# Kernel optimization log

Measured on AMD Instinct MI355X. Metric: run time of the kernel, lower is better.

Reference implementation:

```python
import jax, jax.numpy as jnp
from jax import lax
import numpy as np


def _embed_renorm(table, idx):
    # torch nn.Embedding(max_norm=1): rows with L2 norm > 1 are rescaled to norm 1
    e = table[idx]
    n = jnp.linalg.norm(e, axis=-1, keepdims=True)
    return jnp.where(n > 1.0, e / jnp.maximum(n, 1e-12), e)


def _lstm(x, wih, whh, b, reverse=False):
    # x: [N, T, D]; torch gate order i, f, g, o; zero initial (h, c)
    N, T, _ = x.shape
    H = whh.shape[1]
    xT = jnp.swapaxes(x, 0, 1)  # [T, N, D]
    if reverse:
        xT = xT[::-1]
    pre = jnp.einsum('tnd,gd->tng', xT, wih) + b  # input contribution, [T, N, 4H]

    def step(carry, p):
        h, c = carry
        g = p + h @ whh.T
        i, f, gg, o = jnp.split(g, 4, axis=-1)
        c = jax.nn.sigmoid(f) * c + jax.nn.sigmoid(i) * jnp.tanh(gg)
        h = jax.nn.sigmoid(o) * jnp.tanh(c)
        return (h, c), h

    init = (jnp.zeros((N, H), x.dtype), jnp.zeros((N, H), x.dtype))
    _, hs = lax.scan(step, init, pre)  # [T, N, H]
    if reverse:
        hs = hs[::-1]
    return jnp.swapaxes(hs, 0, 1)  # [N, T, H]


def setup_inputs() -> dict:
    key = jax.random.key(0)
    ks = iter(jax.random.split(key, 32))
    B, W, C = 64, 256, 16
    Vw, Vc, Dw, Dc, H, O = 50000, 100, 256, 64, 512, 3
    s = 0.05  # weight scale to keep LSTM gates in a sane range
    inp = {}
    inp['words'] = jax.random.randint(next(ks), (B, W), 0, Vw)
    inp['chars'] = jax.random.randint(next(ks), (B, W, C), 0, Vc)
    inp['wl_emb'] = jax.random.normal(next(ks), (Vw, Dw), jnp.float32)
    cl_emb = jax.random.normal(next(ks), (Vc, Dc), jnp.float32)
    inp['cl_emb'] = cl_emb.at[0].set(0.0)  # padding_idx=0
    inp['char_wih'] = jax.random.normal(next(ks), (4 * Dc, Dc), jnp.float32) * s
    inp['char_whh'] = jax.random.normal(next(ks), (4 * Dc, Dc), jnp.float32) * s
    inp['char_b'] = jax.random.normal(next(ks), (4 * Dc,), jnp.float32) * s
    for nm in ['l0f', 'l0b']:
        inp[nm + '_wih'] = jax.random.normal(next(ks), (4 * H, Dw + Dc), jnp.float32) * s
        inp[nm + '_whh'] = jax.random.normal(next(ks), (4 * H, H), jnp.float32) * s
        inp[nm + '_b'] = jax.random.normal(next(ks), (4 * H,), jnp.float32) * s
    for nm in ['lf', 'lb']:
        inp[nm + '_wih'] = jax.random.normal(next(ks), (2, 4 * H, 2 * H), jnp.float32) * s
        inp[nm + '_whh'] = jax.random.normal(next(ks), (2, 4 * H, H), jnp.float32) * s
        inp[nm + '_b'] = jax.random.normal(next(ks), (2, 4 * H), jnp.float32) * s
    inp['Wc'] = jax.random.normal(next(ks), (O, 2 * H), jnp.float32) * s
    inp['bc'] = jax.random.normal(next(ks), (O,), jnp.float32) * s
    return inp


def reference(words, chars, wl_emb, cl_emb, char_wih, char_whh, char_b,
              l0f_wih, l0f_whh, l0f_b, l0b_wih, l0b_whh, l0b_b,
              lf_wih, lf_whh, lf_b, lb_wih, lb_whh, lb_b, Wc, bc):
    B, W = words.shape
    C = chars.shape[-1]
    # word-level embeddings
    wl = _embed_renorm(wl_emb, words)  # [B, W, Dw]
    # char-level: batch all B*W ragged words through one LSTM (same math as the
    # per-word python loop: zero-init LSTM per word, take last timestep output)
    ce = _embed_renorm(cl_emb, chars.reshape(B * W, C))  # [B*W, C, Dc]
    ch = _lstm(ce, char_wih, char_whh, char_b)[:, -1, :]  # [B*W, Dc]
    cl = ch.reshape(B, W, -1)
    x = jnp.concatenate([wl, cl], axis=-1)  # [B, W, Dw+Dc]
    # 3-layer bidirectional word LSTM
    h = jnp.concatenate([
        _lstm(x, l0f_wih, l0f_whh, l0f_b),
        _lstm(x, l0b_wih, l0b_whh, l0b_b, reverse=True)], axis=-1)
    for k in range(2):
        h = jnp.concatenate([
            _lstm(h, lf_wih[k], lf_whh[k], lf_b[k]),
            _lstm(h, lb_wih[k], lb_whh[k], lb_b[k], reverse=True)], axis=-1)
    H = h.shape[-1] // 2
    # last_state=True, bi=True: last fwd output + first bwd output
    feat = jnp.concatenate([h[:, -1, :H], h[:, 0, H:]], axis=-1)  # [B, 2H]
    return feat @ Wc.T + bc  # [B, output_size]
```

## Files before the change

### kernel.cpp

```cpp
#include <hip/hip_runtime.h>
#include <math.h>

#define T_   256
#define C_   16

typedef float    f32x4  __attribute__((ext_vector_type(4)));
typedef float    f32x16 __attribute__((ext_vector_type(16)));
typedef _Float16 f16x8  __attribute__((ext_vector_type(8)));
typedef short    short8 __attribute__((ext_vector_type(8)));
typedef unsigned long long ULL;

__device__ __forceinline__ float sigf(float x)  { return 1.0f/(1.0f + __expf(-x)); }
__device__ __forceinline__ float tanhf_(float x){ return 1.0f - 2.0f/(1.0f + __expf(2.0f*x)); }

__device__ __forceinline__ ushort f16b(float w) {
  _Float16 h = (_Float16)w; return __builtin_bit_cast(ushort, h);
}
__device__ __forceinline__ float f16f(ushort b) {
  return (float)__builtin_bit_cast(_Float16, b);
}

#define LLCLD(dst, base, OFF) \
  asm volatile("global_load_dwordx4 %0, %1, off offset:%c2 sc0 sc1" \
               : "=v"(dst) : "v"(base), "n"(OFF) : "memory")

struct PrepArgs {
  const float *cl_emb, *c_wih, *c_b, *c_whh;
  const float *wih[6];
  const float *bb[6];
  ushort *Wh[6];
  float *preT, *whhc, *bP;
  int *barr;
};

__global__ void __launch_bounds__(256) k_prep(PrepArgs A) {
  __shared__ float e[64];
  int b = blockIdx.x, tid = threadIdx.x;
  if (b == 0 && tid < 64) A.barr[tid] = 0;
  if (b < 100) {
    if (tid < 64) e[tid] = A.cl_emb[b*64 + tid];
    __syncthreads();
    float ss = 0.f;
    #pragma unroll 8
    for (int k = 0; k < 64; ++k) ss += e[k]*e[k];
    float nn = sqrtf(ss);
    float scl = (nn > 1.0f) ? 1.0f/nn : 1.0f;
    int u = tid >> 2, q = tid & 3;
    const float* wrow = A.c_wih + (q*64 + u)*64;
    float acc = 0.f;
    #pragma unroll 8
    for (int k = 0; k < 64; ++k) acc += e[k]*wrow[k];
    A.preT[b*256 + tid] = A.c_b[q*64 + u] + scl*acc;
  } else if (b < 164) {
    int i = (b - 100)*256 + tid;
    int k = i >> 8, rem = i & 255, u = rem >> 2, q = rem & 3;
    A.whhc[i] = A.c_whh[(q*64 + u)*64 + k];
  } else if (b < 212) {
    int i = (b - 164)*256 + tid;
    int ld = i >> 11, j = i & 2047, u = j >> 2, q = j & 3;
    A.bP[i] = A.bb[ld][q*512 + u];
  } else {
    int idx = b - 212;
    int ld, off, D;
    if (idx < 1280) { ld = idx / 640; off = idx - ld*640; D = 320; }
    else { idx -= 1280; ld = 2 + (idx >> 11); off = idx & 2047; D = 1024; }
    int i4 = off*256 + tid;
    int D4 = D >> 2;
    int g4 = i4 / D4, k4 = i4 - g4*D4;
    int u = g4 >> 2, q = g4 & 3;
    float4 v = *(const float4*)(A.wih[ld] + (size_t)(q*512 + u)*D + (k4 << 2));
    ushort4 hh;
    hh.x = f16b(v.x); hh.y = f16b(v.y); hh.z = f16b(v.z); hh.w = f16b(v.w);
    *(ushort4*)(A.Wh[ld] + (size_t)g4*D + (k4 << 2)) = hh;
  }
}

__global__ void __launch_bounds__(256) k_wordchar(const int* __restrict__ words,
    const int* __restrict__ chars, const float* __restrict__ wl_emb,
    const float* __restrict__ preT, const float* __restrict__ whhc,
    ushort* __restrict__ Xf) {
  __shared__ float sh[2*64*68];
  int b = blockIdx.x, tid = threadIdx.x;
  if (b >= 256) {
    int tok = b - 256;
    int row = words[tok];
    float e = wl_emb[(size_t)row*256 + tid];
    float ss = e*e;
    #pragma unroll
    for (int o = 32; o; o >>= 1) ss += __shfl_xor(ss, o, 64);
    int lane = tid & 63, wv = tid >> 6;
    if (lane == 0) sh[wv] = ss;
    __syncthreads();
    if (tid == 0) {
      float s2 = sh[0] + sh[1] + sh[2] + sh[3];
      float nn = sqrtf(s2);
      sh[4] = (nn > 1.0f) ? 1.0f/nn : 1.0f;
    }
    __syncthreads();
    Xf[(size_t)tok*320 + tid] = f16b(e*sh[4]);
    return;
  }
  int u = tid & 63, sg = tid >> 6;
  int sbase = b*64 + sg*16;
  float c[16];
  float4 acc[16];
  for (int t = 0; t < C_; ++t) {
    #pragma unroll
    for (int i = 0; i < 16; ++i) {
      int ch = chars[(sbase + i)*C_ + t];
      acc[i] = *(const float4*)(preT + ch*256 + (u << 2));
    }
    if (t > 0) {
      const float* hp = sh + ((t - 1) & 1)*(64*68) + (sg << 4);
      #pragma unroll 2
      for (int k = 0; k < 64; ++k) {
        float4 w = *(const float4*)(whhc + (k << 8) + (u << 2));
        const float* hr = hp + k*68;
        float4 h0 = *(const float4*)(hr + 0);
        float4 h1 = *(const float4*)(hr + 4);
        float4 h2 = *(const float4*)(hr + 8);
        float4 h3 = *(const float4*)(hr + 12);
        float hv[16] = {h0.x,h0.y,h0.z,h0.w, h1.x,h1.y,h1.z,h1.w,
                        h2.x,h2.y,h2.z,h2.w, h3.x,h3.y,h3.z,h3.w};
        #pragma unroll
        for (int i = 0; i < 16; ++i) {
          acc[i].x += w.x*hv[i]; acc[i].y += w.y*hv[i];
          acc[i].z += w.z*hv[i]; acc[i].w += w.w*hv[i];
        }
      }
    }
    float* hw = sh + (t & 1)*(64*68);
    #pragma unroll
    for (int i = 0; i < 16; ++i) {
      float ig = sigf(acc[i].x), fg = sigf(acc[i].y);
      float gg = tanhf_(acc[i].z), og = sigf(acc[i].w);
      float cc = (t == 0) ? (ig*gg) : (fg*c[i] + ig*gg);
      c[i] = cc;
      float hh = og*tanhf_(cc);
      hw[u*68 + (sg << 4) + i] = hh;
      if (t == C_-1) Xf[(size_t)(sbase + i)*320 + 256 + u] = f16b(hh);
    }
    __syncthreads();
  }
}

__global__ void __launch_bounds__(256) k_gemm(const ushort* __restrict__ Xf,
    const ushort* __restrict__ Whf, const ushort* __restrict__ Whb,
    const float* __restrict__ bPf, const float* __restrict__ bPb,
    float* __restrict__ preg, int D, int t0, int TCc) {
  int dir = blockIdx.z;
  const ushort* WhD = dir ? Whb : Whf;
  const float*  bPD = dir ? bPb : bPf;
  int mt = blockIdx.x, nt = blockIdx.y;
  int tid = threadIdx.x;

  __shared__ __align__(16) ushort As[128*64], Bh[128*64];
  int lane = tid & 63, wid = tid >> 6;
  int wm = wid >> 1, wn = wid & 1;
  int l15 = lane & 15, l4 = lane >> 4;

  const ushort *asrc[4], *bhsrc[4];
  ushort *adst[4], *bhdst[4];
  #pragma unroll
  for (int c = 0; c < 4; ++c) {
    int idx = c*256 + tid;
    int row = idx >> 3, ch = idx & 7;
    int chs = ch ^ (row & 7);
    int r = mt*128 + row, s = r >> 6, n = r & 63;
    int ttt = dir ? (T_ - 1 - (t0 + s)) : (t0 + s);
    asrc[c]  = Xf  + ((size_t)n*T_ + ttt)*D + chs*8;
    bhsrc[c] = WhD + (size_t)(nt*128 + row)*D + chs*8;
    adst[c]  = As + idx*8; bhdst[c] = Bh + idx*8;
  }
  int sw = l15 & 7;
  int rA[4], rB[4];
  #pragma unroll
  for (int f = 0; f < 4; ++f) {
    rA[f] = (wm*64 + f*16 + l15) << 6;
    rB[f] = (wn*64 + f*16 + l15) << 6;
  }

  f32x4 acc[4][4];
  #pragma unroll
  for (int a = 0; a < 4; ++a)
    #pragma unroll
    for (int bq = 0; bq < 4; ++bq) acc[a][bq] = (f32x4){0.f,0.f,0.f,0.f};

  for (int k0 = 0; k0 < D; k0 += 64) {
    __syncthreads();
    #pragma unroll
    for (int c = 0; c < 4; ++c) {
      __builtin_amdgcn_global_load_lds(
        (const __attribute__((address_space(1))) void*)(asrc[c] + k0),
        (__attribute__((address_space(3))) void*)adst[c], 16, 0, 0);
      __builtin_amdgcn_global_load_lds(
        (const __attribute__((address_space(1))) void*)(bhsrc[c] + k0),
        (__attribute__((address_space(3))) void*)bhdst[c], 16, 0, 0);
    }
    asm volatile("s_waitcnt vmcnt(0)" ::: "memory");
    __syncthreads();
    #pragma unroll
    for (int ks = 0; ks < 2; ++ks) {
      int fo = (((ks << 2) + l4) ^ sw) << 3;
      f16x8 av[4], bhv[4];
      #pragma unroll
      for (int mf = 0; mf < 4; ++mf)
        av[mf] = __builtin_bit_cast(f16x8, *(const short8*)(As + rA[mf] + fo));
      #pragma unroll
      for (int nf = 0; nf < 4; ++nf)
        bhv[nf] = __builtin_bit_cast(f16x8, *(const short8*)(Bh + rB[nf] + fo));
      #pragma unroll
      for (int mf = 0; mf < 4; ++mf)
        #pragma unroll
        for (int nf = 0; nf < 4; ++nf)
          acc[mf][nf] = __builtin_amdgcn_mfma_f32_16x16x32_f16(av[mf], bhv[nf], acc[mf][nf], 0,0,0);
    }
  }
  float bias[4];
  #pragma unroll
  for (int nf = 0; nf < 4; ++nf) bias[nf] = bPD[nt*128 + wn*64 + nf*16 + l15];
  #pragma unroll
  for (int mf = 0; mf < 4; ++mf)
    #pragma unroll
    for (int nf = 0; nf < 4; ++nf) {
      int g16 = nt*8 + wn*4 + nf;
      #pragma unroll
      for (int rr = 0; rr < 4; ++rr) {
        int r = mt*128 + wm*64 + mf*16 + (l4 << 2) + rr;
        int s = r >> 6, n = r & 63;
        preg[((size_t)(dir*TCc + s)*128 + g16)*1024 + n*16 + l15] = acc[mf][nf][rr] + bias[nf];
      }
    }
}

__global__ void __launch_bounds__(256, 1) k_rec(const float* __restrict__ preg,
    const float* __restrict__ whhf, const float* __restrict__ whhb,
    ushort* __restrict__ XO, ushort* __restrict__ hF, float* __restrict__ cst,
    int* __restrict__ barr, int t0, int TCc, int ebase,
    int doCls, const float* __restrict__ Wc, const float* __restrict__ bc,
    float* __restrict__ outp) {
  __shared__ ushort hs[64*16];
  __shared__ float red[64][4][3];
  int bi = blockIdx.x;
  int dir = bi >> 5, ublk = bi & 31;
  const float* whh = dir ? whhb : whhf;
  int tid = threadIdx.x, w = tid >> 6, l = tid & 63;
  int l31 = l & 31, l5 = l >> 5;
  int gh = w & 1, nh = w >> 1;
  int n_ = nh*32 + l31;
  int q = l31 & 3;
  int urow = ublk*16 + gh*8 + (l31 >> 2);
  int g16b = ublk*4 + gh*2;

  f16x8 ah[32];
  {
    const float* wr = whh + ((size_t)(q*512 + urow))*512 + l5*8;
    #pragma unroll
    for (int ks = 0; ks < 32; ++ks) {
      float4 w0 = *(const float4*)(wr + ks*16);
      float4 w1 = *(const float4*)(wr + ks*16 + 4);
      float wf[8] = {w0.x,w0.y,w0.z,w0.w, w1.x,w1.y,w1.z,w1.w};
      short8 h8;
      #pragma unroll
      for (int j = 0; j < 8; ++j) h8[j] = (short)f16b(wf[j]);
      ah[ks] = __builtin_bit_cast(f16x8, h8);
    }
  }
  float cv[4];
  #pragma unroll
  for (int e = 0; e < 4; ++e) {
    int u = ublk*16 + gh*8 + 2*e + l5;
    cv[e] = (t0 == 0) ? 0.f : cst[(size_t)(dir*64 + n_)*512 + u];
  }
  f32x16 accA;
  {
    const float* pb = preg + (size_t)(dir*TCc)*131072;
    #pragma unroll
    for (int e = 0; e < 4; ++e) {
      f32x4 v = *(const f32x4*)(pb + (g16b + (e>>1))*1024 + n_*16 + 8*(e&1) + 4*l5);
      accA[4*e+0]=v[0]; accA[4*e+1]=v[1]; accA[4*e+2]=v[2]; accA[4*e+3]=v[3];
    }
  }
  int* arrd = barr + dir*32;

  #pragma unroll 1
  for (int s = 0; s < TCc; ++s) {
    int t = t0 + s;
    int tt = dir ? (T_ - 1 - t) : t;
    f32x16 accB = (f32x16)(0.f);
    if (t > 0) {
      const ushort* hb = hF + (size_t)((dir<<1) | ((t-1)&1))*32768 + n_*512 + l5*8;
      f16x8 h0[8], h1[8], h2[8];
      #pragma unroll
      for (int j = 0; j < 8; ++j) LLCLD(h0[j], hb, (0+j)*32);
      #pragma unroll
      for (int j = 0; j < 8; ++j) LLCLD(h1[j], hb, (8+j)*32);
      asm volatile("s_waitcnt vmcnt(8)" ::: "memory");
      __builtin_amdgcn_sched_barrier(0);
      #pragma unroll
      for (int j = 0; j < 8; ++j) LLCLD(h2[j], hb, (16+j)*32);
      #pragma unroll
      for (int j = 0; j < 8; ++j)
        accA = __builtin_amdgcn_mfma_f32_32x32x16_f16(ah[j], h0[j], accA, 0,0,0);
      asm volatile("s_waitcnt vmcnt(8)" ::: "memory");
      __builtin_amdgcn_sched_barrier(0);
      #pragma unroll
      for (int j = 0; j < 8; ++j) LLCLD(h0[j], hb, (24+j)*32);
      #pragma unroll
      for (int j = 0; j < 8; ++j)
        accA = __builtin_amdgcn_mfma_f32_32x32x16_f16(ah[8+j], h1[j], accA, 0,0,0);
      asm volatile("s_waitcnt vmcnt(8)" ::: "memory");
      __builtin_amdgcn_sched_barrier(0);
      #pragma unroll
      for (int j = 0; j < 8; ++j)
        accB = __builtin_amdgcn_mfma_f32_32x32x16_f16(ah[16+j], h2[j], accB, 0,0,0);
      asm volatile("s_waitcnt vmcnt(0)" ::: "memory");
      __builtin_amdgcn_sched_barrier(0);
      #pragma unroll
      for (int j = 0; j < 8; ++j)
        accB = __builtin_amdgcn_mfma_f32_32x32x16_f16(ah[24+j], h0[j], accB, 0,0,0);
    }
    #pragma unroll
    for (int e = 0; e < 4; ++e) {
      float ig = sigf(accA[4*e+0] + accB[4*e+0]);
      float fg = sigf(accA[4*e+1] + accB[4*e+1]);
      float gg = tanhf_(accA[4*e+2] + accB[4*e+2]);
      float og = sigf(accA[4*e+3] + accB[4*e+3]);
      float c = (t == 0) ? (ig*gg) : (fg*cv[e] + ig*gg);
      cv[e] = c;
      float h = og*tanhf_(c);
      int ul = gh*8 + 2*e + l5;
      hs[n_*16 + (ul ^ ((n_&1)<<3))] = f16b(h);
    }
    __syncthreads();
    int n2 = tid >> 2, c2 = tid & 3;
    short4 hv = *(const short4*)&hs[n2*16 + ((c2 ^ ((n2&1)<<1)) << 2)];
    {
      ushort* hdst = hF + (size_t)((dir<<1)|(t&1))*32768 + n2*512 + ublk*16 + c2*4;
      asm volatile("global_store_dwordx2 %0, %1, off sc0 sc1" :: "v"(hdst), "v"(hv) : "memory");
    }
    asm volatile("s_waitcnt vmcnt(0)" ::: "memory");
    __syncthreads();
    int epoch = ebase + s + 1;
    if (tid == 0)
      __hip_atomic_store(&arrd[ublk], epoch, __ATOMIC_RELAXED, __HIP_MEMORY_SCOPE_AGENT);
    if (XO) *(short4*)(XO + (size_t)n2*262144 + (size_t)tt*1024 + dir*512 + ublk*16 + c2*4) = hv;
    if (s + 1 < TCc) {
      const float* pb = preg + (size_t)(dir*TCc + s + 1)*131072;
      #pragma unroll
      for (int e = 0; e < 4; ++e) {
        f32x4 v = *(const f32x4*)(pb + (g16b + (e>>1))*1024 + n_*16 + 8*(e&1) + 4*l5);
        accA[4*e+0]=v[0]; accA[4*e+1]=v[1]; accA[4*e+2]=v[2]; accA[4*e+3]=v[3];
      }
    }
    if (w == 0) {
      bool done = false;
      while (!done) {
        int v = (l < 32) ? __hip_atomic_load(&arrd[l], __ATOMIC_RELAXED, __HIP_MEMORY_SCOPE_AGENT)
                         : 0x7fffffff;
        done = (__ballot(v >= epoch) == ~0ull);
      }
    }
    __syncthreads();
  }
  #pragma unroll
  for (int e = 0; e < 4; ++e)
    cst[(size_t)(dir*64 + n_)*512 + ublk*16 + gh*8 + 2*e + l5] = cv[e];

  if (doCls && bi == 0) {
    int eEnd = ebase + TCc;
    if (w == 0) {
      bool done = false;
      while (!done) {
        int v = (l < 32) ? __hip_atomic_load(&barr[32 + l], __ATOMIC_RELAXED, __HIP_MEMORY_SCOPE_AGENT)
                         : 0x7fffffff;
        done = (__ballot(v >= eEnd) == ~0ull);
      }
    }
    __syncthreads();
    int n = tid >> 2, p = tid & 3;
    const ULL* f0 = (const ULL*)(hF + 32768 + n*512) + p*32;
    const ULL* f1 = (const ULL*)(hF + 3*32768 + n*512) + p*32;
    float p0 = 0.f, p1 = 0.f, p2 = 0.f;
    for (int j8 = 0; j8 < 32; ++j8) {
      ULL v0 = __hip_atomic_load(f0 + j8, __ATOMIC_RELAXED, __HIP_MEMORY_SCOPE_AGENT);
      ULL v1 = __hip_atomic_load(f1 + j8, __ATOMIC_RELAXED, __HIP_MEMORY_SCOPE_AGENT);
      #pragma unroll
      for (int e = 0; e < 4; ++e) {
        int j = p*128 + j8*4 + e;
        float a  = f16f((ushort)(v0 >> (16*e)));
        float b2 = f16f((ushort)(v1 >> (16*e)));
        p0 += a*Wc[j]        + b2*Wc[512 + j];
        p1 += a*Wc[1024 + j] + b2*Wc[1536 + j];
        p2 += a*Wc[2048 + j] + b2*Wc[2560 + j];
      }
    }
    red[n][p][0] = p0; red[n][p][1] = p1; red[n][p][2] = p2;
    __syncthreads();
    if (tid < 192) {
      int nn = tid / 3, o = tid - nn*3;
      outp[nn*3 + o] = red[nn][0][o] + red[nn][1][o] + red[nn][2][o] + red[nn][3][o] + bc[o];
    }
  }
}

extern "C" void kernel_launch(void* const* d_in, const int* in_sizes, int n_in,
                              void* d_out, int out_size, void* d_ws, size_t ws_size,
                              hipStream_t stream) {
  (void)in_sizes; (void)n_in; (void)out_size;
  const int*   words  = (const int*)d_in[0];
  const int*   chars  = (const int*)d_in[1];
  const float* wl_emb = (const float*)d_in[2];
  const float* cl_emb = (const float*)d_in[3];
  const float* c_wih  = (const float*)d_in[4];
  const float* c_whh  = (const float*)d_in[5];
  const float* c_b    = (const float*)d_in[6];
  const float* WIH[6] = {
    (const float*)d_in[7],  (const float*)d_in[10],
    (const float*)d_in[13], (const float*)d_in[16],
    (const float*)d_in[13] + (size_t)2048*1024, (const float*)d_in[16] + (size_t)2048*1024 };
  const float* WHH[3][2] = {
    { (const float*)d_in[8],  (const float*)d_in[11] },
    { (const float*)d_in[14], (const float*)d_in[17] },
    { (const float*)d_in[14] + (size_t)2048*512, (const float*)d_in[17] + (size_t)2048*512 } };
  const float* BB[6] = {
    (const float*)d_in[9],  (const float*)d_in[12],
    (const float*)d_in[15], (const float*)d_in[18],
    (const float*)d_in[15] + 2048, (const float*)d_in[18] + 2048 };
  const float* Wc = (const float*)d_in[19];
  const float* bc = (const float*)d_in[20];

  float* wsp = (float*)d_ws;
  size_t off = 0;
  auto carve = [&](size_t nf) { float* p = wsp + off; off += (nf + 63) & ~(size_t)63; return p; };
  ushort* XA = (ushort*)carve((size_t)16384*1024/2);
  ushort* XB = (ushort*)carve((size_t)16384*1024/2);
  ushort* Wh6[6];
  for (int ld = 0; ld < 6; ++ld) {
    size_t D = (ld < 2) ? 320 : 1024;
    Wh6[ld] = (ushort*)carve((size_t)2048*D/2);
  }
  float* bP   = carve(6*2048);
  float* preT = carve(100*256);
  float* whhc = carve(64*256);
  ushort* hF  = (ushort*)carve((size_t)4*32768/2);
  float* cst  = carve((size_t)2*64*512);
  int* barr   = (int*)carve(64);
  size_t wsFloats = ws_size / 4;
  int TCc = 256;
  while (TCc > 16 && off + (size_t)2*TCc*64*2048 > wsFloats) TCc >>= 1;
  float* preg = carve((size_t)2*TCc*64*2048);
  if (off > wsFloats) return;

  PrepArgs pa;
  pa.cl_emb = cl_emb; pa.c_wih = c_wih; pa.c_b = c_b; pa.c_whh = c_whh;
  for (int ld = 0; ld < 6; ++ld) { pa.wih[ld] = WIH[ld]; pa.bb[ld] = BB[ld];
                                   pa.Wh[ld] = Wh6[ld]; }
  pa.preT = preT; pa.whhc = whhc; pa.bP = bP; pa.barr = barr;
  k_prep<<<9684, 256, 0, stream>>>(pa);

  k_wordchar<<<16640, 256, 0, stream>>>(words, chars, wl_emb, preT, whhc, XA);

  for (int l = 0; l < 3; ++l) {
    const ushort* Xin = (l == 1) ? XB : XA;
    ushort* Xout = (l == 0) ? XB : ((l == 1) ? XA : nullptr);
    int D = l ? 1024 : 320;
    for (int t0 = 0; t0 < T_; t0 += TCc) {
      k_gemm<<<dim3(TCc/2, 16, 2), 256, 0, stream>>>(Xin,
          Wh6[2*l], Wh6[2*l+1],
          bP + (2*l)*2048, bP + (2*l+1)*2048, preg, D, t0, TCc);
      int doCls = (l == 2 && t0 + TCc == T_) ? 1 : 0;
      k_rec<<<64, 256, 0, stream>>>(preg, WHH[l][0], WHH[l][1], Xout, hF, cst,
                                    barr, t0, TCc, l*T_ + t0, doCls, Wc, bc, (float*)d_out);
    }
  }
}
```

Before: 5.938 ms.

## Remap recurrent blocks so each wave syncs independently without LDS or block barriers

Reassigns the recurrent LSTM work so each block owns 8 hidden units for both directions and both batch halves, with each wave handling one (direction, batch-half) group. The LDS staging of h and the two __syncthreads per step are dropped. Lanes pair fp16 outputs through a cross-half shuffle and write 16-byte stores directly, and every wave signals and polls its own 64-entry barrier group. The point is to cut intra-block synchronization and shrink the cross-block barrier critical path. In exchange there are more barrier flags to poll, and the h loads are spread differently across the grid.

```diff
diff --git a/kernel.cpp b/kernel.cpp
--- a/kernel.cpp
+++ b/kernel.cpp
@@ -8,6 +8,7 @@
 typedef float    f32x16 __attribute__((ext_vector_type(16)));
 typedef _Float16 f16x8  __attribute__((ext_vector_type(8)));
 typedef short    short8 __attribute__((ext_vector_type(8)));
+typedef int      i32x4  __attribute__((ext_vector_type(4)));
 typedef unsigned long long ULL;
 
 __device__ __forceinline__ float sigf(float x)  { return 1.0f/(1.0f + __expf(-x)); }
@@ -36,7 +37,7 @@
 __global__ void __launch_bounds__(256) k_prep(PrepArgs A) {
   __shared__ float e[64];
   int b = blockIdx.x, tid = threadIdx.x;
-  if (b == 0 && tid < 64) A.barr[tid] = 0;
+  if (b == 0) A.barr[tid] = 0;
   if (b < 100) {
     if (tid < 64) e[tid] = A.cl_emb[b*64 + tid];
     __syncthreads();
@@ -239,22 +240,20 @@
     int* __restrict__ barr, int t0, int TCc, int ebase,
     int doCls, const float* __restrict__ Wc, const float* __restrict__ bc,
     float* __restrict__ outp) {
-  __shared__ ushort hs[64*16];
   __shared__ float red[64][4][3];
   int bi = blockIdx.x;
-  int dir = bi >> 5, ublk = bi & 31;
+  int tid = threadIdx.x, w = tid >> 6, l = tid & 63;
+  int dir = w >> 1, nh = w & 1;
   const float* whh = dir ? whhb : whhf;
-  int tid = threadIdx.x, w = tid >> 6, l = tid & 63;
   int l31 = l & 31, l5 = l >> 5;
-  int gh = w & 1, nh = w >> 1;
+  int q = l31 & 3, ul = l31 >> 2;
+  int u0 = bi*8;
   int n_ = nh*32 + l31;
-  int q = l31 & 3;
-  int urow = ublk*16 + gh*8 + (l31 >> 2);
-  int g16b = ublk*4 + gh*2;
+  int grp = (dir*2 + nh)*64;
 
   f16x8 ah[32];
   {
-    const float* wr = whh + ((size_t)(q*512 + urow))*512 + l5*8;
+    const float* wr = whh + ((size_t)(q*512 + u0 + ul))*512 + l5*8;
     #pragma unroll
     for (int ks = 0; ks < 32; ++ks) {
       float4 w0 = *(const float4*)(wr + ks*16);
@@ -268,20 +267,18 @@
   }
   float cv[4];
   #pragma unroll
-  for (int e = 0; e < 4; ++e) {
-    int u = ublk*16 + gh*8 + 2*e + l5;
-    cv[e] = (t0 == 0) ? 0.f : cst[(size_t)(dir*64 + n_)*512 + u];
-  }
+  for (int e = 0; e < 4; ++e)
+    cv[e] = (t0 == 0) ? 0.f : cst[(size_t)(dir*64 + n_)*512 + u0 + 2*e + l5];
+
   f32x16 accA;
   {
     const float* pb = preg + (size_t)(dir*TCc)*131072;
     #pragma unroll
     for (int e = 0; e < 4; ++e) {
-      f32x4 v = *(const f32x4*)(pb + (g16b + (e>>1))*1024 + n_*16 + 8*(e&1) + 4*l5);
+      f32x4 v = *(const f32x4*)(pb + (size_t)(bi*2 + (e>>1))*1024 + n_*16 + ((e&1)*2 + l5)*4);
       accA[4*e+0]=v[0]; accA[4*e+1]=v[1]; accA[4*e+2]=v[2]; accA[4*e+3]=v[3];
     }
   }
-  int* arrd = barr + dir*32;
 
   #pragma unroll 1
   for (int s = 0; s < TCc; ++s) {
@@ -289,7 +286,7 @@
     int tt = dir ? (T_ - 1 - t) : t;
     f32x16 accB = (f32x16)(0.f);
     if (t > 0) {
-      const ushort* hb = hF + (size_t)((dir<<1) | ((t-1)&1))*32768 + n_*512 + l5*8;
+      const ushort* hb = hF + (size_t)((dir<<1) | ((t-1)&1))*32768 + (size_t)n_*512 + l5*8;
       f16x8 h0[8], h1[8], h2[8];
       #pragma unroll
       for (int j = 0; j < 8; ++j) LLCLD(h0[j], hb, (0+j)*32);
@@ -320,6 +317,7 @@
       for (int j = 0; j < 8; ++j)
         accB = __builtin_amdgcn_mfma_f32_32x32x16_f16(ah[24+j], h0[j], accB, 0,0,0);
     }
+    uint outw[4];
     #pragma unroll
     for (int e = 0; e < 4; ++e) {
       float ig = sigf(accA[4*e+0] + accB[4*e+0]);
@@ -329,52 +327,53 @@
       float c = (t == 0) ? (ig*gg) : (fg*cv[e] + ig*gg);
       cv[e] = c;
       float h = og*tanhf_(c);
-      int ul = gh*8 + 2*e + l5;
-      hs[n_*16 + (ul ^ ((n_&1)<<3))] = f16b(h);
-    }
-    __syncthreads();
-    int n2 = tid >> 2, c2 = tid & 3;
-    short4 hv = *(const short4*)&hs[n2*16 + ((c2 ^ ((n2&1)<<1)) << 2)];
-    {
-      ushort* hdst = hF + (size_t)((dir<<1)|(t&1))*32768 + n2*512 + ublk*16 + c2*4;
-      asm volatile("global_store_dwordx2 %0, %1, off sc0 sc1" :: "v"(hdst), "v"(hv) : "memory");
+      uint mine = (uint)f16b(h);
+      uint theirs = (uint)__shfl_xor((int)mine, 32, 64);
+      outw[e] = l5 ? ((theirs & 0xffffu) | (mine << 16)) : ((mine & 0xffffu) | (theirs << 16));
+    }
+    if (l5 == 0) {
+      ushort* hdst = hF + (size_t)((dir<<1)|(t&1))*32768 + (size_t)n_*512 + u0;
+      i32x4 vv; vv[0] = (int)outw[0]; vv[1] = (int)outw[1]; vv[2] = (int)outw[2]; vv[3] = (int)outw[3];
+      asm volatile("global_store_dwordx4 %0, %1, off sc0 sc1" :: "v"(hdst), "v"(vv) : "memory");
+    } else if (XO) {
+      uint4 vv; vv.x = outw[0]; vv.y = outw[1]; vv.z = outw[2]; vv.w = outw[3];
+      *(uint4*)(XO + (size_t)n_*262144 + (size_t)tt*1024 + dir*512 + u0) = vv;
     }
     asm volatile("s_waitcnt vmcnt(0)" ::: "memory");
-    __syncthreads();
     int epoch = ebase + s + 1;
-    if (tid == 0)
-      __hip_atomic_store(&arrd[ublk], epoch, __ATOMIC_RELAXED, __HIP_MEMORY_SCOPE_AGENT);
-    if (XO) *(short4*)(XO + (size_t)n2*262144 + (size_t)tt*1024 + dir*512 + ublk*16 + c2*4) = hv;
+    if (l == 0)
+      __hip_atomic_store(&barr[grp + bi], epoch, __ATOMIC_RELAXED, __HIP_MEMORY_SCOPE_AGENT);
     if (s + 1 < TCc) {
       const float* pb = preg + (size_t)(dir*TCc + s + 1)*131072;
       #pragma unroll
       for (int e = 0; e < 4; ++e) {
-        f32x4 v = *(const f32x4*)(pb + (g16b + (e>>1))*1024 + n_*16 + 8*(e&1) + 4*l5);
+        f32x4 v = *(const f32x4*)(pb + (size_t)(bi*2 + (e>>1))*1024 + n_*16 + ((e&1)*2 + l5)*4);
         accA[4*e+0]=v[0]; accA[4*e+1]=v[1]; accA[4*e+2]=v[2]; accA[4*e+3]=v[3];
       }
     }
-    if (w == 0) {
+    {
       bool done = false;
       while (!done) {
-        int v = (l < 32) ? __hip_atomic_load(&arrd[l], __ATOMIC_RELAXED, __HIP_MEMORY_SCOPE_AGENT)
-                         : 0x7fffffff;
+        int v = __hip_atomic_load(&barr[grp + l], __ATOMIC_RELAXED, __HIP_MEMORY_SCOPE_AGENT);
         done = (__ballot(v >= epoch) == ~0ull);
       }
     }
-    __syncthreads();
   }
   #pragma unroll
   for (int e = 0; e < 4; ++e)
-    cst[(size_t)(dir*64 + n_)*512 + ublk*16 + gh*8 + 2*e + l5] = cv[e];
+    cst[(size_t)(dir*64 + n_)*512 + u0 + 2*e + l5] = cv[e];
 
   if (doCls && bi == 0) {
     int eEnd = ebase + TCc;
     if (w == 0) {
       bool done = false;
       while (!done) {
-        int v = (l < 32) ? __hip_atomic_load(&barr[32 + l], __ATOMIC_RELAXED, __HIP_MEMORY_SCOPE_AGENT)
-                         : 0x7fffffff;
-        done = (__ballot(v >= eEnd) == ~0ull);
+        int v0 = __hip_atomic_load(&barr[l],       __ATOMIC_RELAXED, __HIP_MEMORY_SCOPE_AGENT);
+        int v1 = __hip_atomic_load(&barr[64 + l],  __ATOMIC_RELAXED, __HIP_MEMORY_SCOPE_AGENT);
+        int v2 = __hip_atomic_load(&barr[128 + l], __ATOMIC_RELAXED, __HIP_MEMORY_SCOPE_AGENT);
+        int v3 = __hip_atomic_load(&barr[192 + l], __ATOMIC_RELAXED, __HIP_MEMORY_SCOPE_AGENT);
+        bool ok = (v0 >= eEnd) && (v1 >= eEnd) && (v2 >= eEnd) && (v3 >= eEnd);
+        done = (__ballot(ok) == ~0ull);
       }
     }
     __syncthreads();
@@ -445,7 +444,7 @@
   float* whhc = carve(64*256);
   ushort* hF  = (ushort*)carve((size_t)4*32768/2);
   float* cst  = carve((size_t)2*64*512);
-  int* barr   = (int*)carve(64);
+  int* barr   = (int*)carve(256);
   size_t wsFloats = ws_size / 4;
   int TCc = 256;
   while (TCc > 16 && off + (size_t)2*TCc*64*2048 > wsFloats) TCc >>= 1;
```

After: 7.491 ms. +26.1%, slower.
